# Performance work log

Hardware: AMD Instinct MI355X
Metric: run time of the kernel (lower is better)

The kernel has to match this reference:

```python
import jax, jax.numpy as jnp
import numpy as np

N_ATOMS = 262144          # 2**18 atoms
N_PAIRS = 16777216        # 2**24 pairs (~64 neighbors/atom)
SIGMA = 1.0
EPSILON = 1.0
CUTOFF = 2.5              # 2.5 * sigma (module default)


def setup_inputs() -> dict:
    key = jax.random.key(0)
    k_pos, k_i, k_off = jax.random.split(key, 3)
    # Gaussian cloud, scale 2 -> typical pair distances O(1-5), many inside cutoff
    positions = 2.0 * jax.random.normal(k_pos, (N_ATOMS, 3), dtype=jnp.float32)
    # Large box; shifts are zero so cell does not alter displacements
    cell = 100.0 * jnp.eye(3, dtype=jnp.float32)
    # Neighbor-list style pairs; guarantee j != i so distances are strictly > 0
    i = jax.random.randint(k_i, (N_PAIRS,), 0, N_ATOMS, dtype=jnp.int32)
    off = jax.random.randint(k_off, (N_PAIRS,), 1, N_ATOMS, dtype=jnp.int32)
    j = (i + off) % N_ATOMS
    mapping = jnp.stack([i, j])  # [2, n_pairs]
    shifts = jnp.zeros((N_PAIRS, 3), dtype=jnp.float32)
    return {"positions": positions, "cell": cell, "mapping": mapping, "shifts": shifts}


def reference(positions, cell, mapping, shifts):
    # Gather pair displacements: dr = r_j - r_i + shifts @ cell (row-vector cell)
    i, j = mapping[0], mapping[1]
    dr_vec = positions[j] - positions[i] + shifts @ cell      # [P, 3]
    distances = jnp.sqrt(jnp.sum(dr_vec * dr_vec, axis=-1))   # [P]

    # Lennard-Jones 12-6 pair energy: 4 eps ((s/r)^12 - (s/r)^6)
    sr6 = (SIGMA / distances) ** 6
    sr12 = sr6 * sr6
    pair_energies = 4.0 * EPSILON * (sr12 - sr6)
    mask = distances < CUTOFF
    pair_energies = jnp.where(mask, pair_energies, 0.0)
    energy = 0.5 * jnp.sum(pair_energies)

    # Pair force magnitude: 24 eps / r * (2 (s/r)^12 - (s/r)^6)
    pair_forces = 24.0 * EPSILON / distances * (2.0 * sr12 - sr6)
    pair_forces = jnp.where(mask, pair_forces, 0.0)
    force_vectors = (pair_forces / distances)[:, None] * dr_vec  # [P, 3]

    # Scatter-add back to atoms: -fv at i, +fv at j
    forces = (jnp.zeros_like(positions)
              .at[i].add(-force_vectors)
              .at[j].add(force_vectors))
    return energy, forces
```

## Files before the change

### kernel.cpp

```cpp
#include <hip/hip_runtime.h>

#define N_ATOMS 262144
#define N_PAIRS 16777216
#define FCOMP (N_ATOMS * 3)

#define NB      256
#define BSHIFT  10
#define ALOCAL  (N_ATOMS / NB)
#define CAPBB   32
#define SC_THREADS 256
#define NPT     32
#define PPB     (SC_THREADS * NPT)
#define G_TOTAL (N_PAIRS / PPB)
#define LLIST_CAP 3072
#define ACC_THREADS 1024

typedef int          v4i __attribute__((ext_vector_type(4)));
typedef float        v4f __attribute__((ext_vector_type(4)));
typedef unsigned int u32;
typedef u32          v4u __attribute__((ext_vector_type(4)));


__device__ __forceinline__ void atomic_add_f32(float* addr, float v) {
    unsafeAtomicAdd(addr, v);
}
__device__ __forceinline__ float scrub_nonfinite(float x) {
    return ((__float_as_uint(x) & 0x7f800000u) == 0x7f800000u) ? 0.0f : x;
}

__global__ void __launch_bounds__(256) lj_prep_kernel(
    const float* __restrict__ pos, v4f* __restrict__ pos4,
    float* __restrict__ forces, double* __restrict__ ews)
{
    const int a = blockIdx.x * blockDim.x + threadIdx.x;
    if (a < N_ATOMS) {
        v4f p = {pos[3 * a + 0], pos[3 * a + 1], pos[3 * a + 2], 0.0f};
        pos4[a] = p;
        forces[3 * a + 0] = 0.0f;
        forces[3 * a + 1] = 0.0f;
        forces[3 * a + 2] = 0.0f;
    }
    if (a == 0) *ews = 0.0;
}

__global__ void __launch_bounds__(SC_THREADS) lj_scatter_kernel(
    const v4f* __restrict__ pos4,
    const float* __restrict__ cell,
    const int* __restrict__ map_i,
    const int* __restrict__ map_j,
    const float* __restrict__ shifts,
    v4u* __restrict__ records,
    u32* __restrict__ cnts,
    int pair_base, int g_count,
    double* __restrict__ energy_ws)
{
    __shared__ u32 hist[NB];
    __shared__ u32 nlist;
    __shared__ v4u list[LLIST_CAP];
    __shared__ double wave_sums[SC_THREADS / 64];

    const int tid = threadIdx.x;
    const int g   = blockIdx.x;
    if (tid < NB) hist[tid] = 0;
    if (tid == 0) nlist = 0;
    __syncthreads();

    const float c00 = cell[0], c01 = cell[1], c02 = cell[2];
    const float c10 = cell[3], c11 = cell[4], c12 = cell[5];
    const float c20 = cell[6], c21 = cell[7], c22 = cell[8];

    double e_acc = 0.0;

    auto do_pair = [&](int i, int j, float sx, float sy, float sz) {
        const float shx = sx * c00 + sy * c10 + sz * c20;
        const float shy = sx * c01 + sy * c11 + sz * c21;
        const float shz = sx * c02 + sy * c12 + sz * c22;
        const v4f Pi = pos4[i];
        const v4f Pj = pos4[j];
        const float dx = Pj.x - Pi.x + shx;
        const float dy = Pj.y - Pi.y + shy;
        const float dz = Pj.z - Pi.z + shz;
        const float r2 = dx * dx + dy * dy + dz * dz;
        if (r2 < 6.25f) {
            const float inv_r2 = 1.0f / r2;
            const float sr6  = inv_r2 * inv_r2 * inv_r2;
            const float sr12 = sr6 * sr6;
            e_acc += (double)scrub_nonfinite(4.0f * (sr12 - sr6));
            const float pf = 24.0f * inv_r2 * (2.0f * sr12 - sr6);
            const float fx = scrub_nonfinite(pf * dx);
            const float fy = scrub_nonfinite(pf * dy);
            const float fz = scrub_nonfinite(pf * dz);
            const u32 idx = atomicAdd(&nlist, 2u);
            if (idx + 1 < LLIST_CAP) {
                v4u ri = {(u32)i, __float_as_uint(-fx), __float_as_uint(-fy), __float_as_uint(-fz)};
                v4u rj = {(u32)j, __float_as_uint( fx), __float_as_uint( fy), __float_as_uint( fz)};
                list[idx]     = ri;
                list[idx + 1] = rj;
                atomicAdd(&hist[((u32)i) >> BSHIFT], 1u);
                atomicAdd(&hist[((u32)j) >> BSHIFT], 1u);
            }
        }
    };

    const int base4 = pair_base / 4;
    #pragma unroll
    for (int s = 0; s < NPT / 4; ++s) {
        const int e = base4 + (s * g_count + g) * SC_THREADS + tid;
        const v4i mi = ((const v4i*)map_i)[e];
        const v4i mj = ((const v4i*)map_j)[e];
        const v4f sa = ((const v4f*)shifts)[3 * e + 0];
        const v4f sb = ((const v4f*)shifts)[3 * e + 1];
        const v4f sc = ((const v4f*)shifts)[3 * e + 2];
        do_pair(mi.x, mj.x, sa.x, sa.y, sa.z);
        do_pair(mi.y, mj.y, sa.w, sb.x, sb.y);
        do_pair(mi.z, mj.z, sb.z, sb.w, sc.x);
        do_pair(mi.w, mj.w, sc.y, sc.z, sc.w);
    }
    __syncthreads();

    if (tid < NB) {
        const u32 c = hist[tid];
        cnts[(size_t)g * NB + tid] = (c < CAPBB) ? c : (u32)CAPBB;
        hist[tid] = 0;
    }
    __syncthreads();

    const u32 n = (nlist < (u32)LLIST_CAP) ? nlist : (u32)LLIST_CAP;
    for (u32 t = tid; t < n; t += SC_THREADS) {
        const v4u rec = list[t];
        const u32 b = rec.x >> BSHIFT;
        const u32 slot = atomicAdd(&hist[b], 1u);
        if (slot < CAPBB)
            records[((size_t)g * NB + b) * CAPBB + slot] = rec;
    }

    for (int off = 32; off > 0; off >>= 1)
        e_acc += __shfl_down(e_acc, off, 64);
    const int lane = tid & 63, wid = tid >> 6;
    if (lane == 0) wave_sums[wid] = e_acc;
    __syncthreads();
    if (tid == 0) {
        double s = 0.0;
        for (int w = 0; w < SC_THREADS / 64; ++w) s += wave_sums[w];
        atomicAdd(energy_ws, s);
    }
}

__global__ void __launch_bounds__(ACC_THREADS) lj_accum_kernel(
    const v4u* __restrict__ records,
    const u32* __restrict__ cnts,
    int g_count,
    float* __restrict__ forces)
{
    __shared__ float facc[ALOCAL * 3];
    __shared__ u32 lcnt[G_TOTAL];
    const int b = blockIdx.x;
    const int tid = threadIdx.x;

    for (int t = tid; t < ALOCAL * 3; t += ACC_THREADS) facc[t] = 0.0f;
    for (int t = tid; t < g_count; t += ACC_THREADS) lcnt[t] = cnts[(size_t)t * NB + b];
    __syncthreads();

    const int total = g_count * CAPBB;
    for (int r = tid; r < total; r += ACC_THREADS) {
        const int g = r >> 5;
        const int k = r & (CAPBB - 1);
        if ((u32)k < lcnt[g]) {
            const v4u rec = records[((size_t)g * NB + b) * CAPBB + k];
            const u32 al = rec.x & (ALOCAL - 1);
            atomicAdd(&facc[al * 3 + 0], __uint_as_float(rec.y));
            atomicAdd(&facc[al * 3 + 1], __uint_as_float(rec.z));
            atomicAdd(&facc[al * 3 + 2], __uint_as_float(rec.w));
        }
    }
    __syncthreads();

    const int fbase = (b << BSHIFT) * 3;
    for (int t = tid; t < ALOCAL * 3; t += ACC_THREADS)
        forces[fbase + t] += facc[t];
}

__global__ void __launch_bounds__(256) lj_zero_kernel(float* __restrict__ buf, int n,
                                                      double* __restrict__ ews) {
    int idx = blockIdx.x * blockDim.x + threadIdx.x;
    int stride = gridDim.x * blockDim.x;
    for (int k = idx; k < n; k += stride) buf[k] = 0.0f;
    if (idx == 0) *ews = 0.0;
}

__global__ void __launch_bounds__(256) lj_pair_direct_kernel(
    const float* __restrict__ pos,
    const float* __restrict__ cell,
    const int* __restrict__ map_i,
    const int* __restrict__ map_j,
    const float* __restrict__ shifts,
    float* __restrict__ forces,
    double* __restrict__ energy_ws)
{
    const float c00 = cell[0], c01 = cell[1], c02 = cell[2];
    const float c10 = cell[3], c11 = cell[4], c12 = cell[5];
    const float c20 = cell[6], c21 = cell[7], c22 = cell[8];
    double e_acc = 0.0;
    const int t = blockIdx.x * blockDim.x + threadIdx.x;
    const v4i mi = ((const v4i*)map_i)[t];
    const v4i mj = ((const v4i*)map_j)[t];
    const v4f sa = ((const v4f*)shifts)[3 * t + 0];
    const v4f sb = ((const v4f*)shifts)[3 * t + 1];
    const v4f sc = ((const v4f*)shifts)[3 * t + 2];
    auto body = [&](int i, int j, float sx, float sy, float sz) {
        const float shx = sx * c00 + sy * c10 + sz * c20;
        const float shy = sx * c01 + sy * c11 + sz * c21;
        const float shz = sx * c02 + sy * c12 + sz * c22;
        const float dx = pos[3*j]   - pos[3*i]   + shx;
        const float dy = pos[3*j+1] - pos[3*i+1] + shy;
        const float dz = pos[3*j+2] - pos[3*i+2] + shz;
        const float r2 = dx*dx + dy*dy + dz*dz;
        if (r2 < 6.25f) {
            const float inv_r2 = 1.0f / r2;
            const float sr6 = inv_r2*inv_r2*inv_r2, sr12 = sr6*sr6;
            e_acc += (double)scrub_nonfinite(4.0f * (sr12 - sr6));
            const float pf = 24.0f * inv_r2 * (2.0f * sr12 - sr6);
            const float fx = scrub_nonfinite(pf*dx), fy = scrub_nonfinite(pf*dy), fz = scrub_nonfinite(pf*dz);
            atomic_add_f32(&forces[3*i+0], -fx); atomic_add_f32(&forces[3*i+1], -fy); atomic_add_f32(&forces[3*i+2], -fz);
            atomic_add_f32(&forces[3*j+0],  fx); atomic_add_f32(&forces[3*j+1],  fy); atomic_add_f32(&forces[3*j+2],  fz);
        }
    };
    body(mi.x, mj.x, sa.x, sa.y, sa.z);
    body(mi.y, mj.y, sa.w, sb.x, sb.y);
    body(mi.z, mj.z, sb.z, sb.w, sc.x);
    body(mi.w, mj.w, sc.y, sc.z, sc.w);
    for (int off = 32; off > 0; off >>= 1) e_acc += __shfl_down(e_acc, off, 64);
    __shared__ double ws4[4];
    if ((threadIdx.x & 63) == 0) ws4[threadIdx.x >> 6] = e_acc;
    __syncthreads();
    if (threadIdx.x == 0) atomicAdd(energy_ws, ws4[0] + ws4[1] + ws4[2] + ws4[3]);
}

__global__ void __launch_bounds__(256) lj_scrub_kernel(float* __restrict__ buf, int n) {
    int idx = blockIdx.x * blockDim.x + threadIdx.x;
    int stride = gridDim.x * blockDim.x;
    for (int k = idx; k < n; k += stride) buf[k] = scrub_nonfinite(buf[k]);
}

__global__ void lj_finalize_kernel(float* __restrict__ out, const double* __restrict__ ews) {
    out[0] = scrub_nonfinite((float)(0.5 * *ews));
}

extern "C" void kernel_launch(void* const* d_in, const int* in_sizes, int n_in,
                              void* d_out, int out_size, void* d_ws, size_t ws_size,
                              hipStream_t stream) {
    const float* positions = (const float*)d_in[0];
    const float* cell      = (const float*)d_in[1];
    const int*   map_i     = (const int*)d_in[2];
    const int*   map_j     = map_i + N_PAIRS;
    const float* shifts    = (const float*)d_in[3];

    float*  out    = (float*)d_out;
    float*  forces = out + 1;
    double* ews    = (double*)d_ws;
    v4f*    pos4   = (v4f*)((char*)d_ws + 64);

    int C = 0;
    {
        const int cands[6] = {1, 2, 4, 8, 16, 32};
        for (int ci = 0; ci < 6; ++ci) {
            const int c = cands[ci];
            const size_t gc = G_TOTAL / c;
            const size_t need = 64 + (size_t)N_ATOMS * 16
                              + gc * NB * 4
                              + gc * NB * CAPBB * 16;
            if (need <= ws_size) { C = c; break; }
        }
    }

    if (C > 0) {
        const int gc = G_TOTAL / C;
        const int pc = N_PAIRS / C;
        u32* cnts    = (u32*)((char*)d_ws + 64 + (size_t)N_ATOMS * 16);
        v4u* records = (v4u*)((char*)cnts + (size_t)gc * NB * 4);

        lj_prep_kernel<<<N_ATOMS / 256, 256, 0, stream>>>(positions, pos4, forces, ews);
        for (int c = 0; c < C; ++c) {
            lj_scatter_kernel<<<gc, SC_THREADS, 0, stream>>>(
                pos4, cell, map_i, map_j, shifts, records, cnts, c * pc, gc, ews);
            lj_accum_kernel<<<NB, ACC_THREADS, 0, stream>>>(records, cnts, gc, forces);
        }
        lj_scrub_kernel<<<1024, 256, 0, stream>>>(forces, FCOMP);
    } else {
        lj_zero_kernel<<<2048, 256, 0, stream>>>(forces, FCOMP, ews);
        lj_pair_direct_kernel<<<N_PAIRS / 4 / 256, 256, 0, stream>>>(
            positions, cell, map_i, map_j, shifts, forces, ews);
        lj_scrub_kernel<<<1024, 256, 0, stream>>>(forces, FCOMP);
    }
    lj_finalize_kernel<<<1, 1, 0, stream>>>(out, ews);
}
```

Baseline: 386.2 us.

## Write bucketed force records directly to global, dropping the LDS staging list

The scatter kernel no longer stages pair records in a 48KB shared-memory list and then re-buckets them. Each in-cutoff pair now takes a slot from the shared histogram and writes its two records straight to the per-bucket global slots with nontemporal stores. Input mapping and shift loads also become nontemporal, and launch bounds ask for 7 blocks per CU, which the smaller LDS footprint makes possible. This removes the LDS round trip and the second pass and raises occupancy. In exchange, global writes become scattered per pair rather than grouped per bucket, which may hurt write coalescing.

```diff
diff --git a/kernel.cpp b/kernel.cpp
--- a/kernel.cpp
+++ b/kernel.cpp
@@ -12,7 +12,6 @@
 #define NPT     32
 #define PPB     (SC_THREADS * NPT)
 #define G_TOTAL (N_PAIRS / PPB)
-#define LLIST_CAP 3072
 #define ACC_THREADS 1024
 
 typedef int          v4i __attribute__((ext_vector_type(4)));
@@ -43,7 +42,7 @@
     if (a == 0) *ews = 0.0;
 }
 
-__global__ void __launch_bounds__(SC_THREADS) lj_scatter_kernel(
+__global__ void __launch_bounds__(SC_THREADS, 7) lj_scatter_kernel(
     const v4f* __restrict__ pos4,
     const float* __restrict__ cell,
     const int* __restrict__ map_i,
@@ -55,14 +54,11 @@
     double* __restrict__ energy_ws)
 {
     __shared__ u32 hist[NB];
-    __shared__ u32 nlist;
-    __shared__ v4u list[LLIST_CAP];
     __shared__ double wave_sums[SC_THREADS / 64];
 
     const int tid = threadIdx.x;
     const int g   = blockIdx.x;
     if (tid < NB) hist[tid] = 0;
-    if (tid == 0) nlist = 0;
     __syncthreads();
 
     const float c00 = cell[0], c01 = cell[1], c02 = cell[2];
@@ -70,6 +66,7 @@
     const float c20 = cell[6], c21 = cell[7], c22 = cell[8];
 
     double e_acc = 0.0;
+    const size_t rec_base = (size_t)g * NB * CAPBB;
 
     auto do_pair = [&](int i, int j, float sx, float sy, float sz) {
         const float shx = sx * c00 + sy * c10 + sz * c20;
@@ -90,14 +87,17 @@
             const float fx = scrub_nonfinite(pf * dx);
             const float fy = scrub_nonfinite(pf * dy);
             const float fz = scrub_nonfinite(pf * dz);
-            const u32 idx = atomicAdd(&nlist, 2u);
-            if (idx + 1 < LLIST_CAP) {
+            const u32 bi = ((u32)i) >> BSHIFT;
+            const u32 bj = ((u32)j) >> BSHIFT;
+            const u32 si = atomicAdd(&hist[bi], 1u);
+            if (si < CAPBB) {
                 v4u ri = {(u32)i, __float_as_uint(-fx), __float_as_uint(-fy), __float_as_uint(-fz)};
-                v4u rj = {(u32)j, __float_as_uint( fx), __float_as_uint( fy), __float_as_uint( fz)};
-                list[idx]     = ri;
-                list[idx + 1] = rj;
-                atomicAdd(&hist[((u32)i) >> BSHIFT], 1u);
-                atomicAdd(&hist[((u32)j) >> BSHIFT], 1u);
+                __builtin_nontemporal_store(ri, &records[rec_base + (size_t)bi * CAPBB + si]);
+            }
+            const u32 sj = atomicAdd(&hist[bj], 1u);
+            if (sj < CAPBB) {
+                v4u rj = {(u32)j, __float_as_uint(fx), __float_as_uint(fy), __float_as_uint(fz)};
+                __builtin_nontemporal_store(rj, &records[rec_base + (size_t)bj * CAPBB + sj]);
             }
         }
     };
@@ -106,11 +106,11 @@
     #pragma unroll
     for (int s = 0; s < NPT / 4; ++s) {
         const int e = base4 + (s * g_count + g) * SC_THREADS + tid;
-        const v4i mi = ((const v4i*)map_i)[e];
-        const v4i mj = ((const v4i*)map_j)[e];
-        const v4f sa = ((const v4f*)shifts)[3 * e + 0];
-        const v4f sb = ((const v4f*)shifts)[3 * e + 1];
-        const v4f sc = ((const v4f*)shifts)[3 * e + 2];
+        const v4i mi = __builtin_nontemporal_load(((const v4i*)map_i) + e);
+        const v4i mj = __builtin_nontemporal_load(((const v4i*)map_j) + e);
+        const v4f sa = __builtin_nontemporal_load(((const v4f*)shifts) + 3 * e + 0);
+        const v4f sb = __builtin_nontemporal_load(((const v4f*)shifts) + 3 * e + 1);
+        const v4f sc = __builtin_nontemporal_load(((const v4f*)shifts) + 3 * e + 2);
         do_pair(mi.x, mj.x, sa.x, sa.y, sa.z);
         do_pair(mi.y, mj.y, sa.w, sb.x, sb.y);
         do_pair(mi.z, mj.z, sb.z, sb.w, sc.x);
@@ -121,17 +121,6 @@
     if (tid < NB) {
         const u32 c = hist[tid];
         cnts[(size_t)g * NB + tid] = (c < CAPBB) ? c : (u32)CAPBB;
-        hist[tid] = 0;
-    }
-    __syncthreads();
-
-    const u32 n = (nlist < (u32)LLIST_CAP) ? nlist : (u32)LLIST_CAP;
-    for (u32 t = tid; t < n; t += SC_THREADS) {
-        const v4u rec = list[t];
-        const u32 b = rec.x >> BSHIFT;
-        const u32 slot = atomicAdd(&hist[b], 1u);
-        if (slot < CAPBB)
-            records[((size_t)g * NB + b) * CAPBB + slot] = rec;
     }
 
     for (int off = 32; off > 0; off >>= 1)
```

Result: slower. 463.8 us (+20.1%).
